# Performance work log

Measured on AMD Instinct MI355X. Metric: run time of the kernel, lower is better.

## Reference

```python
import jax, jax.numpy as jnp
import numpy as np

N_NODES = 20000
N_EDGES = 320000
D = 128  # d_edge = d_node = d_global


def setup_inputs() -> dict:
    key = jax.random.key(0)
    ks = jax.random.split(key, 8)
    inv = lambda fan_in: 1.0 / np.sqrt(fan_in)
    return {
        "edge_attr": jax.random.normal(ks[0], (N_EDGES, D), dtype=jnp.float32),
        "node_attr": jax.random.normal(ks[1], (N_NODES, D), dtype=jnp.float32),
        "u": jax.random.normal(ks[2], (D,), dtype=jnp.float32),
        "senders": jax.random.randint(ks[3], (N_EDGES,), 0, N_NODES, dtype=jnp.int32),
        "receivers": jax.random.randint(ks[4], (N_EDGES,), 0, N_NODES, dtype=jnp.int32),
        "We": jax.random.normal(ks[5], (4 * D, D), dtype=jnp.float32) * inv(4 * D),
        "be": jnp.zeros((D,), dtype=jnp.float32),
        "Wv": jax.random.normal(ks[6], (3 * D, D), dtype=jnp.float32) * inv(3 * D),
        "bv": jnp.zeros((D,), dtype=jnp.float32),
        "Wu": jax.random.normal(ks[7], (3 * D, D), dtype=jnp.float32) * inv(3 * D),
        "bu": jnp.zeros((D,), dtype=jnp.float32),
    }


def reference(edge_attr, node_attr, u, senders, receivers, We, be, Wv, bv, Wu, bu):
    E = edge_attr.shape[0]
    N = node_attr.shape[0]
    u_e = jnp.broadcast_to(u, (E, u.shape[0]))
    u_v = jnp.broadcast_to(u, (N, u.shape[0]))

    # Edge block: phi_e(e, v_r, v_s, u) -- gather endpoint features per edge
    e_in = jnp.concatenate(
        [edge_attr, node_attr[receivers], node_attr[senders], u_e], axis=-1
    )  # [E, 4D]
    e_new = jax.nn.relu(e_in @ We + be)  # [E, D]

    # rho_ev: sum incoming edges per receiver node (scatter-add)
    aggr_e = jax.ops.segment_sum(e_new, receivers, num_segments=N)  # [N, D]

    # Node block: phi_v(aggr_e, v, u)
    v_in = jnp.concatenate([aggr_e, node_attr, u_v], axis=-1)  # [N, 3D]
    v_new = jax.nn.relu(v_in @ Wv + bv)  # [N, D]

    # Global block: rho_eu / rho_vu = mean, phi_u(aggr_e, aggr_v, u)
    aggr_e_u = jnp.mean(e_new, axis=0)
    aggr_v_u = jnp.mean(v_new, axis=0)
    u_in = jnp.concatenate([aggr_e_u, aggr_v_u, u], axis=-1)  # [3D]
    u_new = jax.nn.relu(u_in @ Wu + bu)  # [D]

    return e_new, v_new, u_new
```

## Files before the change

### kernel.cpp

```cpp
#include <hip/hip_runtime.h>
#include <hip/hip_bf16.h>


#define NN 20000
#define NE 320000
#define DD 128
#define SAS 136
#define SBS 136

typedef unsigned short u16;
typedef __attribute__((ext_vector_type(8))) short bf16x8;
typedef __attribute__((ext_vector_type(4))) float f32x4;

__device__ __forceinline__ float b2f(unsigned short h) {
  return __uint_as_float(((unsigned int)h) << 16);
}
__device__ __forceinline__ unsigned short f2b(float f) {
  unsigned int u = __float_as_uint(f);
  unsigned int r = (u + 0x7fffu + ((u >> 16) & 1u)) >> 16;
  return (unsigned short)r;
}

__global__ void k_const(const float* u, const float* We, const float* be,
                        const float* Wv, const float* bv, float* ce,
                        float* cv) {
  __shared__ float su[DD];
  int j = threadIdx.x;
  su[j] = u[j];
  __syncthreads();
  float a = be[j];
  float b = bv[j];
  for (int k = 0; k < DD; ++k) {
    a = fmaf(su[k], We[(384 + k) * DD + j], a);
    b = fmaf(su[k], Wv[(256 + k) * DD + j], b);
  }
  ce[j] = a;
  cv[j] = b;
}

__global__ void k_prep(const float* We, const float* Wv, u16* wt) {
  int m = blockIdx.x;
  const float* W = (m == 0)   ? We
                   : (m == 1) ? We + 128 * DD
                   : (m == 2) ? We + 256 * DD
                   : (m == 3) ? Wv + 128 * DD
                              : Wv;
  u16* o = wt + (size_t)m * DD * DD;
  for (int i = threadIdx.x; i < DD * DD; i += 256) {
    int k = i >> 7, n = i & 127;
    o[n * DD + k] = f2b(W[i]);
  }
}

__global__ void k_hist(const int* recv, int* counts) {
  int e = blockIdx.x * blockDim.x + threadIdx.x;
  if (e < NE) atomicAdd(&counts[recv[e]], 1);
}

__global__ void k_scan(const int* counts, int* rowptr, int* cursor) {
  __shared__ int wsum[16];
  __shared__ int carry;
  int tid = threadIdx.x;
  int lane = tid & 63, wv = tid >> 6;
  if (tid == 0) carry = 0;
  __syncthreads();
  for (int base = 0; base < NN; base += 1024) {
    int i = base + tid;
    int v = (i < NN) ? counts[i] : 0;
    int x = v;
    for (int off = 1; off < 64; off <<= 1) {
      int t = __shfl_up(x, off);
      if (lane >= off) x += t;
    }
    if (lane == 63) wsum[wv] = x;
    __syncthreads();
    if (wv == 0 && lane < 16) {
      int y = wsum[lane];
      for (int off = 1; off < 16; off <<= 1) {
        int t = __shfl_up(y, off);
        if (lane >= off) y += t;
      }
      wsum[lane] = y;
    }
    __syncthreads();
    int woff = (wv > 0) ? wsum[wv - 1] : 0;
    int excl = carry + woff + (x - v);
    if (i < NN) {
      rowptr[i] = excl;
      cursor[i] = excl;
    }
    __syncthreads();
    if (tid == 0) carry += wsum[15];
    __syncthreads();
  }
  if (tid == 0) rowptr[NN] = carry;
}

__global__ void k_fill(const int* recv, int* cursor, int* elist) {
  int e = blockIdx.x * blockDim.x + threadIdx.x;
  if (e < NE) {
    int slot = atomicAdd(&cursor[recv[e]], 1);
    elist[slot] = e;
  }
}

__device__ __forceinline__ void mfma_core(const u16* sA, const u16* sBT,
                                          int lane, int w, f32x4 acc[4][2]) {
  int r15 = lane & 15;
  int koff = (lane >> 4) * 8;
#pragma unroll
  for (int k0 = 0; k0 < DD; k0 += 32) {
    bf16x8 a[4], b[2];
#pragma unroll
    for (int mt = 0; mt < 4; ++mt)
      a[mt] = *(const bf16x8*)&sA[(mt * 16 + r15) * SAS + k0 + koff];
#pragma unroll
    for (int nt = 0; nt < 2; ++nt)
      b[nt] = *(const bf16x8*)&sBT[(w * 32 + nt * 16 + r15) * SBS + k0 + koff];
#pragma unroll
    for (int mt = 0; mt < 4; ++mt)
#pragma unroll
      for (int nt = 0; nt < 2; ++nt)
        acc[mt][nt] = __builtin_amdgcn_mfma_f32_16x16x32_bf16(
            a[mt], b[nt], acc[mt][nt], 0, 0, 0);
  }
}

__device__ __forceinline__ void stage_w(u16* sBT, const u16* wsrc, int tid) {
  const uint4* ws = (const uint4*)wsrc;
  for (int i = tid; i < DD * DD / 8; i += 256) {
    int n = i >> 4, kk = (i & 15) * 8;
    *(uint4*)&sBT[n * SBS + kk] = ws[i];
  }
}

__global__ __launch_bounds__(256) void k_edge(const float* edge_attr,
                                              const u16* wt, const int* recv,
                                              const int* send, const u16* P,
                                              const float* ce, float* e_out,
                                              float* sum_e) {
  __shared__ __align__(16) u16 sA[64 * SAS];
  __shared__ __align__(16) u16 sBT[DD * SBS];
  __shared__ int sRecv[64], sSend[64];
  __shared__ float sCol[DD];
  int tid = threadIdx.x;
  int e0 = blockIdx.x * 64;
  stage_w(sBT, wt, tid);
  const float4* src = (const float4*)(edge_attr + (size_t)e0 * DD);
  for (int i = tid; i < 64 * DD / 4; i += 256) {
    float4 a4 = src[i];
    int rr = i >> 5, cc = (i & 31) * 4;
    ushort4 h;
    h.x = f2b(a4.x); h.y = f2b(a4.y); h.z = f2b(a4.z); h.w = f2b(a4.w);
    *(ushort4*)&sA[rr * SAS + cc] = h;
  }
  if (tid < 64) {
    sRecv[tid] = recv[e0 + tid];
    sSend[tid] = send[e0 + tid];
  }
  if (tid < DD) sCol[tid] = 0.f;
  __syncthreads();
  int lane = tid & 63, w = tid >> 6;
  f32x4 acc[4][2] = {};
  mfma_core(sA, sBT, lane, w, acc);
  int c15 = lane & 15, quad = lane >> 4;
  int col0 = w * 32 + c15, col1 = col0 + 16;
  float ce0 = ce[col0], ce1 = ce[col1];
  float cs0 = 0.f, cs1 = 0.f;
#pragma unroll
  for (int mt = 0; mt < 4; ++mt) {
#pragma unroll
    for (int r = 0; r < 4; ++r) {
      int m = mt * 16 + quad * 4 + r;
      int rc = sRecv[m], sd = sSend[m];
      const u16* p1 = &P[(size_t)rc * 384];
      const u16* p2 = &P[(size_t)sd * 384 + 128];
      float v0 = fmaxf(acc[mt][0][r] + b2f(p1[col0]) + b2f(p2[col0]) + ce0, 0.f);
      float v1 = fmaxf(acc[mt][1][r] + b2f(p1[col1]) + b2f(p2[col1]) + ce1, 0.f);
      size_t ob = (size_t)(e0 + m) * DD;
      e_out[ob + col0] = v0;
      e_out[ob + col1] = v1;
      cs0 += v0;
      cs1 += v1;
    }
  }
  atomicAdd(&sCol[col0], cs0);
  atomicAdd(&sCol[col1], cs1);
  __syncthreads();
  if (tid < DD) atomicAdd(&sum_e[tid], sCol[tid]);
}

__global__ __launch_bounds__(256) void k_nodeproj(const float* node_attr,
                                                  const u16* wt, u16* P) {
  __shared__ __align__(16) u16 sA[64 * SAS];
  __shared__ __align__(16) u16 sBT[DD * SBS];
  int tid = threadIdx.x;
  int n0 = blockIdx.x * 64;
  int sel = blockIdx.y;
  stage_w(sBT, wt + (size_t)(1 + sel) * DD * DD, tid);
  for (int i = tid; i < 64 * DD / 4; i += 256) {
    int rr = i >> 5, cc = (i & 31) * 4;
    float4 a4 = (n0 + rr < NN)
                    ? ((const float4*)node_attr)[(size_t)(n0 + rr) * 32 + (i & 31)]
                    : make_float4(0, 0, 0, 0);
    ushort4 h;
    h.x = f2b(a4.x); h.y = f2b(a4.y); h.z = f2b(a4.z); h.w = f2b(a4.w);
    *(ushort4*)&sA[rr * SAS + cc] = h;
  }
  __syncthreads();
  int lane = tid & 63, w = tid >> 6;
  f32x4 acc[4][2] = {};
  mfma_core(sA, sBT, lane, w, acc);
  int c15 = lane & 15, quad = lane >> 4;
  int col0 = w * 32 + c15, col1 = col0 + 16;
#pragma unroll
  for (int mt = 0; mt < 4; ++mt) {
#pragma unroll
    for (int r = 0; r < 4; ++r) {
      int n = n0 + mt * 16 + quad * 4 + r;
      if (n < NN) {
        u16* o = &P[(size_t)n * 384 + sel * 128];
        o[col0] = f2b(acc[mt][0][r]);
        o[col1] = f2b(acc[mt][1][r]);
      }
    }
  }
}

__global__ __launch_bounds__(256) void k_aggr(const float* e_new,
                                              const int* rowptr,
                                              const int* elist, float* aggr) {
  int tid = threadIdx.x;
  int wv = tid >> 6, lane = tid & 63;
  int n = blockIdx.x * 4 + wv;
  if (n >= NN) return;
  int b = rowptr[n], e = rowptr[n + 1];
  float sx = 0.f, sy = 0.f, tx = 0.f, ty = 0.f;
  int i = b;
  for (; i + 1 < e; i += 2) {
    int e1 = elist[i], e2 = elist[i + 1];
    float2 a = *(const float2*)&e_new[(size_t)e1 * DD + lane * 2];
    float2 c = *(const float2*)&e_new[(size_t)e2 * DD + lane * 2];
    sx += a.x; sy += a.y; tx += c.x; ty += c.y;
  }
  if (i < e) {
    float2 a = *(const float2*)&e_new[(size_t)elist[i] * DD + lane * 2];
    sx += a.x; sy += a.y;
  }
  float2 out;
  out.x = sx + tx;
  out.y = sy + ty;
  *(float2*)&aggr[(size_t)n * DD + lane * 2] = out;
}

__global__ __launch_bounds__(256) void k_node(const float* aggr, const u16* wt,
                                              const u16* P, const float* cv,
                                              float* v_out, float* sum_v) {
  __shared__ __align__(16) u16 sA[64 * SAS];
  __shared__ __align__(16) u16 sBT[DD * SBS];
  __shared__ float sCol[DD];
  int tid = threadIdx.x;
  int n0 = blockIdx.x * 64;
  stage_w(sBT, wt + (size_t)4 * DD * DD, tid);
  for (int i = tid; i < 64 * DD / 4; i += 256) {
    int rr = i >> 5, cc = (i & 31) * 4;
    float4 a4 = (n0 + rr < NN)
                    ? ((const float4*)aggr)[(size_t)(n0 + rr) * 32 + (i & 31)]
                    : make_float4(0, 0, 0, 0);
    ushort4 h;
    h.x = f2b(a4.x); h.y = f2b(a4.y); h.z = f2b(a4.z); h.w = f2b(a4.w);
    *(ushort4*)&sA[rr * SAS + cc] = h;
  }
  if (tid < DD) sCol[tid] = 0.f;
  __syncthreads();
  int lane = tid & 63, w = tid >> 6;
  f32x4 acc[4][2] = {};
  mfma_core(sA, sBT, lane, w, acc);
  int c15 = lane & 15, quad = lane >> 4;
  int col0 = w * 32 + c15, col1 = col0 + 16;
  float cv0 = cv[col0], cv1 = cv[col1];
  float cs0 = 0.f, cs1 = 0.f;
#pragma unroll
  for (int mt = 0; mt < 4; ++mt) {
#pragma unroll
    for (int r = 0; r < 4; ++r) {
      int n = n0 + mt * 16 + quad * 4 + r;
      if (n < NN) {
        const u16* pv = &P[(size_t)n * 384 + 256];
        float v0 = fmaxf(acc[mt][0][r] + b2f(pv[col0]) + cv0, 0.f);
        float v1 = fmaxf(acc[mt][1][r] + b2f(pv[col1]) + cv1, 0.f);
        size_t ob = (size_t)n * DD;
        v_out[ob + col0] = v0;
        v_out[ob + col1] = v1;
        cs0 += v0;
        cs1 += v1;
      }
    }
  }
  atomicAdd(&sCol[col0], cs0);
  atomicAdd(&sCol[col1], cs1);
  __syncthreads();
  if (tid < DD) atomicAdd(&sum_v[tid], sCol[tid]);
}

__global__ void k_global(const float* sumbuf, const float* u, const float* Wu,
                         const float* bu, float* out) {
  __shared__ float sin_[384];
  int j = threadIdx.x;
  sin_[j] = sumbuf[j] * (1.0f / (float)NE);
  sin_[128 + j] = sumbuf[128 + j] * (1.0f / (float)NN);
  sin_[256 + j] = u[j];
  __syncthreads();
  float a = bu[j];
  for (int k = 0; k < 384; ++k) a = fmaf(sin_[k], Wu[k * DD + j], a);
  out[j] = fmaxf(a, 0.f);
}

extern "C" void kernel_launch(void* const* d_in, const int* in_sizes, int n_in,
                              void* d_out, int out_size, void* d_ws,
                              size_t ws_size, hipStream_t stream) {
  const float* edge_attr = (const float*)d_in[0];
  const float* node_attr = (const float*)d_in[1];
  const float* u = (const float*)d_in[2];
  const int* senders = (const int*)d_in[3];
  const int* receivers = (const int*)d_in[4];
  const float* We = (const float*)d_in[5];
  const float* be = (const float*)d_in[6];
  const float* Wv = (const float*)d_in[7];
  const float* bv = (const float*)d_in[8];
  const float* Wu = (const float*)d_in[9];
  const float* bu = (const float*)d_in[10];

  float* e_out = (float*)d_out;
  float* v_out = e_out + (size_t)NE * DD;
  float* u_out = v_out + (size_t)NN * DD;

  int* counts = (int*)d_ws;
  float* sumbuf = (float*)d_ws + NN;
  int* rowptr = (int*)d_ws + NN + 256;
  int* cursor = rowptr + NN + 1;
  int* elist = cursor + NN;
  size_t off = (size_t)(NN + 256 + (NN + 1) + NN + NE);
  off = (off + 3) & ~(size_t)3;
  u16* wt = (u16*)((float*)d_ws + off);
  u16* P = wt + (size_t)5 * DD * DD;
  float* ce = (float*)(P + (size_t)NN * 384);
  float* cv = ce + 128;
  float* aggr = cv + 128;

  hipMemsetAsync(d_ws, 0, (size_t)(NN + 256) * 4, stream);
  k_prep<<<5, 256, 0, stream>>>(We, Wv, wt);
  k_const<<<1, 128, 0, stream>>>(u, We, be, Wv, bv, ce, cv);
  k_hist<<<NE / 256, 256, 0, stream>>>(receivers, counts);
  k_scan<<<1, 1024, 0, stream>>>(counts, rowptr, cursor);
  k_fill<<<NE / 256, 256, 0, stream>>>(receivers, cursor, elist);
  k_nodeproj<<<dim3((NN + 63) / 64, 3), 256, 0, stream>>>(node_attr, wt, P);
  k_edge<<<NE / 64, 256, 0, stream>>>(edge_attr, wt, receivers, senders, P, ce,
                                      e_out, sumbuf);
  k_aggr<<<(NN + 3) / 4, 256, 0, stream>>>(e_out, rowptr, elist, aggr);
  k_node<<<(NN + 63) / 64, 256, 0, stream>>>(aggr, wt, P, cv, v_out,
                                             sumbuf + 128);
  k_global<<<1, 128, 0, stream>>>(sumbuf, u, Wu, bu, u_out);
}
```

Measured before the change: 570.3 us.

## Fuse edge aggregation into persistent receiver-sorted edge kernel and merge setup launches

The edge kernel becomes persistent with a fixed grid. It processes edges in receiver-sorted order through the CSR edge list, prefetching the next tile's gathered inputs into registers while the current tile runs its MFMAs. Segment sums are accumulated as run-length reductions per receiver with global atomics, which removes the separate aggregation pass that re-read all of e_out. Setup, histogram, fill and node-projection launches are merged into fewer kernels. The trade-offs are gathered, non-contiguous edge_attr reads and e_out writes, float atomics that make the sums order-nondeterministic, aggregation of bf16-rounded edge values, and a larger memset for the aggr buffer.

Result: faster. 519.3 us (-9.0%).

```diff
diff --git a/kernel.cpp b/kernel.cpp
--- a/kernel.cpp
+++ b/kernel.cpp
@@ -7,6 +7,8 @@
 #define DD 128
 #define SAS 136
 #define SBS 136
+#define NBLK 768
+#define NTILE 5000
 
 typedef unsigned short u16;
 typedef __attribute__((ext_vector_type(8))) short bf16x8;
@@ -21,40 +23,70 @@
   return (unsigned short)r;
 }
 
-__global__ void k_const(const float* u, const float* We, const float* be,
-                        const float* Wv, const float* bv, float* ce,
-                        float* cv) {
+__device__ __forceinline__ void mfma_core(const u16* sA, const u16* sBT,
+                                          int lane, int w, f32x4 acc[4][2]) {
+  int r15 = lane & 15;
+  int koff = (lane >> 4) * 8;
+#pragma unroll
+  for (int k0 = 0; k0 < DD; k0 += 32) {
+    bf16x8 a[4], b[2];
+#pragma unroll
+    for (int mt = 0; mt < 4; ++mt)
+      a[mt] = *(const bf16x8*)&sA[(mt * 16 + r15) * SAS + k0 + koff];
+#pragma unroll
+    for (int nt = 0; nt < 2; ++nt)
+      b[nt] = *(const bf16x8*)&sBT[(w * 32 + nt * 16 + r15) * SBS + k0 + koff];
+#pragma unroll
+    for (int mt = 0; mt < 4; ++mt)
+#pragma unroll
+      for (int nt = 0; nt < 2; ++nt)
+        acc[mt][nt] = __builtin_amdgcn_mfma_f32_16x16x32_bf16(
+            a[mt], b[nt], acc[mt][nt], 0, 0, 0);
+  }
+}
+
+__device__ __forceinline__ void stage_w(u16* sBT, const u16* wsrc, int tid) {
+  const uint4* ws = (const uint4*)wsrc;
+  for (int i = tid; i < DD * DD / 8; i += 256) {
+    int n = i >> 4, kk = (i & 15) * 8;
+    *(uint4*)&sBT[n * SBS + kk] = ws[i];
+  }
+}
+
+__global__ __launch_bounds__(256) void k_setup(const int* recv, int* counts,
+                                               const float* We, const float* Wv,
+                                               const float* u, const float* be,
+                                               const float* bv, u16* wt,
+                                               float* ce, float* cv) {
   __shared__ float su[DD];
-  int j = threadIdx.x;
-  su[j] = u[j];
-  __syncthreads();
-  float a = be[j];
-  float b = bv[j];
-  for (int k = 0; k < DD; ++k) {
-    a = fmaf(su[k], We[(384 + k) * DD + j], a);
-    b = fmaf(su[k], Wv[(256 + k) * DD + j], b);
-  }
-  ce[j] = a;
-  cv[j] = b;
-}
-
-__global__ void k_prep(const float* We, const float* Wv, u16* wt) {
-  int m = blockIdx.x;
-  const float* W = (m == 0)   ? We
-                   : (m == 1) ? We + 128 * DD
-                   : (m == 2) ? We + 256 * DD
-                   : (m == 3) ? Wv + 128 * DD
-                              : Wv;
-  u16* o = wt + (size_t)m * DD * DD;
-  for (int i = threadIdx.x; i < DD * DD; i += 256) {
-    int k = i >> 7, n = i & 127;
-    o[n * DD + k] = f2b(W[i]);
-  }
-}
-
-__global__ void k_hist(const int* recv, int* counts) {
-  int e = blockIdx.x * blockDim.x + threadIdx.x;
-  if (e < NE) atomicAdd(&counts[recv[e]], 1);
+  int b = blockIdx.x, tid = threadIdx.x;
+  if (b < 1250) {
+    atomicAdd(&counts[recv[b * 256 + tid]], 1);
+  } else if (b < 1255) {
+    int m = b - 1250;
+    const float* W = (m == 0)   ? We
+                     : (m == 1) ? We + 128 * DD
+                     : (m == 2) ? We + 256 * DD
+                     : (m == 3) ? Wv + 128 * DD
+                                : Wv;
+    u16* o = wt + (size_t)m * DD * DD;
+    for (int i = tid; i < DD * DD; i += 256) {
+      int k = i >> 7, n = i & 127;
+      o[n * DD + k] = f2b(W[i]);
+    }
+  } else {
+    if (tid < DD) su[tid] = u[tid];
+    __syncthreads();
+    if (tid < DD) {
+      float a = be[tid], c = bv[tid];
+      for (int k = 0; k < DD; ++k) {
+        a = fmaf(su[k], We[(384 + k) * DD + tid], a);
+        c = fmaf(su[k], Wv[(256 + k) * DD + tid], c);
+      }
+      ce[tid] = a;
+      cv[tid] = c;
+    }
+  }
 }
 
 __global__ void k_scan(const int* counts, int* rowptr, int* cursor) {
@@ -96,108 +128,19 @@
   if (tid == 0) rowptr[NN] = carry;
 }
 
-__global__ void k_fill(const int* recv, int* cursor, int* elist) {
-  int e = blockIdx.x * blockDim.x + threadIdx.x;
-  if (e < NE) {
+__global__ __launch_bounds__(256) void k_mid(const int* recv, int* cursor,
+                                             int* elist, const float* node_attr,
+                                             const u16* wt, u16* P) {
+  __shared__ __align__(16) u16 sA[64 * SAS];
+  __shared__ __align__(16) u16 sBT[DD * SBS];
+  int b = blockIdx.x, tid = threadIdx.x;
+  if (b < 1250) {
+    int e = b * 256 + tid;
     int slot = atomicAdd(&cursor[recv[e]], 1);
     elist[slot] = e;
-  }
-}
-
-__device__ __forceinline__ void mfma_core(const u16* sA, const u16* sBT,
-                                          int lane, int w, f32x4 acc[4][2]) {
-  int r15 = lane & 15;
-  int koff = (lane >> 4) * 8;
-#pragma unroll
-  for (int k0 = 0; k0 < DD; k0 += 32) {
-    bf16x8 a[4], b[2];
-#pragma unroll
-    for (int mt = 0; mt < 4; ++mt)
-      a[mt] = *(const bf16x8*)&sA[(mt * 16 + r15) * SAS + k0 + koff];
-#pragma unroll
-    for (int nt = 0; nt < 2; ++nt)
-      b[nt] = *(const bf16x8*)&sBT[(w * 32 + nt * 16 + r15) * SBS + k0 + koff];
-#pragma unroll
-    for (int mt = 0; mt < 4; ++mt)
-#pragma unroll
-      for (int nt = 0; nt < 2; ++nt)
-        acc[mt][nt] = __builtin_amdgcn_mfma_f32_16x16x32_bf16(
-            a[mt], b[nt], acc[mt][nt], 0, 0, 0);
-  }
-}
-
-__device__ __forceinline__ void stage_w(u16* sBT, const u16* wsrc, int tid) {
-  const uint4* ws = (const uint4*)wsrc;
-  for (int i = tid; i < DD * DD / 8; i += 256) {
-    int n = i >> 4, kk = (i & 15) * 8;
-    *(uint4*)&sBT[n * SBS + kk] = ws[i];
-  }
-}
-
-__global__ __launch_bounds__(256) void k_edge(const float* edge_attr,
-                                              const u16* wt, const int* recv,
-                                              const int* send, const u16* P,
-                                              const float* ce, float* e_out,
-                                              float* sum_e) {
-  __shared__ __align__(16) u16 sA[64 * SAS];
-  __shared__ __align__(16) u16 sBT[DD * SBS];
-  __shared__ int sRecv[64], sSend[64];
-  __shared__ float sCol[DD];
-  int tid = threadIdx.x;
-  int e0 = blockIdx.x * 64;
-  stage_w(sBT, wt, tid);
-  const float4* src = (const float4*)(edge_attr + (size_t)e0 * DD);
-  for (int i = tid; i < 64 * DD / 4; i += 256) {
-    float4 a4 = src[i];
-    int rr = i >> 5, cc = (i & 31) * 4;
-    ushort4 h;
-    h.x = f2b(a4.x); h.y = f2b(a4.y); h.z = f2b(a4.z); h.w = f2b(a4.w);
-    *(ushort4*)&sA[rr * SAS + cc] = h;
-  }
-  if (tid < 64) {
-    sRecv[tid] = recv[e0 + tid];
-    sSend[tid] = send[e0 + tid];
-  }
-  if (tid < DD) sCol[tid] = 0.f;
-  __syncthreads();
-  int lane = tid & 63, w = tid >> 6;
-  f32x4 acc[4][2] = {};
-  mfma_core(sA, sBT, lane, w, acc);
-  int c15 = lane & 15, quad = lane >> 4;
-  int col0 = w * 32 + c15, col1 = col0 + 16;
-  float ce0 = ce[col0], ce1 = ce[col1];
-  float cs0 = 0.f, cs1 = 0.f;
-#pragma unroll
-  for (int mt = 0; mt < 4; ++mt) {
-#pragma unroll
-    for (int r = 0; r < 4; ++r) {
-      int m = mt * 16 + quad * 4 + r;
-      int rc = sRecv[m], sd = sSend[m];
-      const u16* p1 = &P[(size_t)rc * 384];
-      const u16* p2 = &P[(size_t)sd * 384 + 128];
-      float v0 = fmaxf(acc[mt][0][r] + b2f(p1[col0]) + b2f(p2[col0]) + ce0, 0.f);
-      float v1 = fmaxf(acc[mt][1][r] + b2f(p1[col1]) + b2f(p2[col1]) + ce1, 0.f);
-      size_t ob = (size_t)(e0 + m) * DD;
-      e_out[ob + col0] = v0;
-      e_out[ob + col1] = v1;
-      cs0 += v0;
-      cs1 += v1;
-    }
-  }
-  atomicAdd(&sCol[col0], cs0);
-  atomicAdd(&sCol[col1], cs1);
-  __syncthreads();
-  if (tid < DD) atomicAdd(&sum_e[tid], sCol[tid]);
-}
-
-__global__ __launch_bounds__(256) void k_nodeproj(const float* node_attr,
-                                                  const u16* wt, u16* P) {
-  __shared__ __align__(16) u16 sA[64 * SAS];
-  __shared__ __align__(16) u16 sBT[DD * SBS];
-  int tid = threadIdx.x;
-  int n0 = blockIdx.x * 64;
-  int sel = blockIdx.y;
-  stage_w(sBT, wt + (size_t)(1 + sel) * DD * DD, tid);
+    return;
+  }
+  int n0 = (b - 1250) * 64;
   for (int i = tid; i < 64 * DD / 4; i += 256) {
     int rr = i >> 5, cc = (i & 31) * 4;
     float4 a4 = (n0 + rr < NN)
@@ -207,50 +150,158 @@
     h.x = f2b(a4.x); h.y = f2b(a4.y); h.z = f2b(a4.z); h.w = f2b(a4.w);
     *(ushort4*)&sA[rr * SAS + cc] = h;
   }
-  __syncthreads();
   int lane = tid & 63, w = tid >> 6;
-  f32x4 acc[4][2] = {};
-  mfma_core(sA, sBT, lane, w, acc);
   int c15 = lane & 15, quad = lane >> 4;
   int col0 = w * 32 + c15, col1 = col0 + 16;
-#pragma unroll
-  for (int mt = 0; mt < 4; ++mt) {
-#pragma unroll
-    for (int r = 0; r < 4; ++r) {
-      int n = n0 + mt * 16 + quad * 4 + r;
-      if (n < NN) {
-        u16* o = &P[(size_t)n * 384 + sel * 128];
-        o[col0] = f2b(acc[mt][0][r]);
-        o[col1] = f2b(acc[mt][1][r]);
-      }
-    }
-  }
-}
-
-__global__ __launch_bounds__(256) void k_aggr(const float* e_new,
-                                              const int* rowptr,
-                                              const int* elist, float* aggr) {
+  for (int sel = 0; sel < 3; ++sel) {
+    __syncthreads();
+    stage_w(sBT, wt + (size_t)(1 + sel) * DD * DD, tid);
+    __syncthreads();
+    f32x4 acc[4][2] = {};
+    mfma_core(sA, sBT, lane, w, acc);
+#pragma unroll
+    for (int mt = 0; mt < 4; ++mt)
+#pragma unroll
+      for (int r = 0; r < 4; ++r) {
+        int n = n0 + mt * 16 + quad * 4 + r;
+        if (n < NN) {
+          u16* o = &P[(size_t)n * 384 + sel * 128];
+          o[col0] = f2b(acc[mt][0][r]);
+          o[col1] = f2b(acc[mt][1][r]);
+        }
+      }
+  }
+}
+
+__global__ __launch_bounds__(256) void k_edge(const float* edge_attr,
+                                              const u16* wt, const int* elist,
+                                              const int* recv, const int* send,
+                                              const u16* P, const float* ce,
+                                              float* e_out, float* aggr,
+                                              float* sum_e) {
+  __shared__ __align__(16) u16 sBT[DD * SBS];
+  __shared__ __align__(16) u16 sAO[64 * SAS];
+  __shared__ int sEid[64], sRecv[64], sSend[64];
   int tid = threadIdx.x;
-  int wv = tid >> 6, lane = tid & 63;
-  int n = blockIdx.x * 4 + wv;
-  if (n >= NN) return;
-  int b = rowptr[n], e = rowptr[n + 1];
-  float sx = 0.f, sy = 0.f, tx = 0.f, ty = 0.f;
-  int i = b;
-  for (; i + 1 < e; i += 2) {
-    int e1 = elist[i], e2 = elist[i + 1];
-    float2 a = *(const float2*)&e_new[(size_t)e1 * DD + lane * 2];
-    float2 c = *(const float2*)&e_new[(size_t)e2 * DD + lane * 2];
-    sx += a.x; sy += a.y; tx += c.x; ty += c.y;
-  }
-  if (i < e) {
-    float2 a = *(const float2*)&e_new[(size_t)elist[i] * DD + lane * 2];
-    sx += a.x; sy += a.y;
-  }
-  float2 out;
-  out.x = sx + tx;
-  out.y = sy + ty;
-  *(float2*)&aggr[(size_t)n * DD + lane * 2] = out;
+  int lane = tid & 63, w = tid >> 6;
+  int r15 = lane & 15, quad = lane >> 4;
+  int col0 = w * 32 + r15, col1 = col0 + 16;
+  int myrow = tid >> 5;
+  int mycol = (tid & 31) * 4;
+
+  float4 areg[8];
+  int eid8[8];
+  int eidN = 0, rcN = 0, sdN = 0;
+  int t = blockIdx.x;
+
+  {
+    int base = t * 64;
+#pragma unroll
+    for (int j = 0; j < 8; ++j) eid8[j] = elist[base + myrow + 8 * j];
+    if (tid < 64) {
+      eidN = elist[base + tid];
+      rcN = recv[eidN];
+      sdN = send[eidN];
+    }
+#pragma unroll
+    for (int j = 0; j < 8; ++j)
+      areg[j] = *(const float4*)&edge_attr[(size_t)eid8[j] * DD + mycol];
+  }
+  stage_w(sBT, wt, tid);
+  float ce0 = ce[col0], ce1 = ce[col1];
+  float colsum = 0.f;
+  bool first = true;
+
+  for (; t < NTILE; t += NBLK) {
+    if (!first) __syncthreads();
+    first = false;
+#pragma unroll
+    for (int j = 0; j < 8; ++j) {
+      ushort4 h;
+      h.x = f2b(areg[j].x); h.y = f2b(areg[j].y);
+      h.z = f2b(areg[j].z); h.w = f2b(areg[j].w);
+      *(ushort4*)&sAO[(myrow + 8 * j) * SAS + mycol] = h;
+    }
+    if (tid < 64) {
+      sEid[tid] = eidN;
+      sRecv[tid] = rcN;
+      sSend[tid] = sdN;
+    }
+    __syncthreads();
+    int tn = t + NBLK;
+    if (tn < NTILE) {
+      int base = tn * 64;
+#pragma unroll
+      for (int j = 0; j < 8; ++j) eid8[j] = elist[base + myrow + 8 * j];
+      if (tid < 64) {
+        eidN = elist[base + tid];
+        rcN = recv[eidN];
+        sdN = send[eidN];
+      }
+#pragma unroll
+      for (int j = 0; j < 8; ++j)
+        areg[j] = *(const float4*)&edge_attr[(size_t)eid8[j] * DD + mycol];
+    }
+    f32x4 acc[4][2] = {};
+    mfma_core(sAO, sBT, lane, w, acc);
+    float vv[4][2][4];
+#pragma unroll
+    for (int mt = 0; mt < 4; ++mt)
+#pragma unroll
+      for (int r = 0; r < 4; ++r) {
+        int m = mt * 16 + quad * 4 + r;
+        const u16* p1 = &P[(size_t)sRecv[m] * 384];
+        const u16* p2 = &P[(size_t)sSend[m] * 384 + 128];
+        vv[mt][0][r] =
+            fmaxf(acc[mt][0][r] + b2f(p1[col0]) + b2f(p2[col0]) + ce0, 0.f);
+        vv[mt][1][r] =
+            fmaxf(acc[mt][1][r] + b2f(p1[col1]) + b2f(p2[col1]) + ce1, 0.f);
+      }
+    __syncthreads();
+    u16* sOutH = sAO;
+#pragma unroll
+    for (int mt = 0; mt < 4; ++mt)
+#pragma unroll
+      for (int r = 0; r < 4; ++r) {
+        int m = mt * 16 + quad * 4 + r;
+        sOutH[m * SAS + col0] = f2b(vv[mt][0][r]);
+        sOutH[m * SAS + col1] = f2b(vv[mt][1][r]);
+      }
+    __syncthreads();
+    if (tid < DD) {
+      float run = 0.f;
+      int prev = sRecv[0];
+      for (int r = 0; r < 64; ++r) {
+        int cur = sRecv[r];
+        float v = b2f(sOutH[r * SAS + tid]);
+        if (cur != prev) {
+          atomicAdd(&aggr[(size_t)prev * DD + tid], run);
+          run = 0.f;
+          prev = cur;
+        }
+        run += v;
+        colsum += v;
+      }
+      atomicAdd(&aggr[(size_t)prev * DD + tid], run);
+    } else {
+      int tt = tid - 128;
+#pragma unroll
+      for (int j = 0; j < 8; ++j) {
+        int i = tt + 128 * j;
+        int row = i >> 4, ch = (i & 15) * 8;
+        uint4 q = *(const uint4*)&sOutH[row * SAS + ch];
+        float4 f0, f1;
+        f0.x = b2f((u16)(q.x & 0xffff)); f0.y = b2f((u16)(q.x >> 16));
+        f0.z = b2f((u16)(q.y & 0xffff)); f0.w = b2f((u16)(q.y >> 16));
+        f1.x = b2f((u16)(q.z & 0xffff)); f1.y = b2f((u16)(q.z >> 16));
+        f1.z = b2f((u16)(q.w & 0xffff)); f1.w = b2f((u16)(q.w >> 16));
+        float* dst = &e_out[(size_t)sEid[row] * DD + ch];
+        *(float4*)dst = f0;
+        *(float4*)(dst + 4) = f1;
+      }
+    }
+  }
+  if (tid < DD) atomicAdd(&sum_e[tid], colsum);
 }
 
 __global__ __launch_bounds__(256) void k_node(const float* aggr, const u16* wt,
@@ -281,7 +332,7 @@
   float cv0 = cv[col0], cv1 = cv[col1];
   float cs0 = 0.f, cs1 = 0.f;
 #pragma unroll
-  for (int mt = 0; mt < 4; ++mt) {
+  for (int mt = 0; mt < 4; ++mt)
 #pragma unroll
     for (int r = 0; r < 4; ++r) {
       int n = n0 + mt * 16 + quad * 4 + r;
@@ -296,7 +347,6 @@
         cs1 += v1;
       }
     }
-  }
   atomicAdd(&sCol[col0], cs0);
   atomicAdd(&sCol[col1], cs1);
   __syncthreads();
@@ -337,27 +387,25 @@
 
   int* counts = (int*)d_ws;
   float* sumbuf = (float*)d_ws + NN;
-  int* rowptr = (int*)d_ws + NN + 256;
+  float* aggr = (float*)d_ws + NN + 256;
+  int* rowptr = (int*)d_ws + NN + 256 + NN * DD;
   int* cursor = rowptr + NN + 1;
   int* elist = cursor + NN;
-  size_t off = (size_t)(NN + 256 + (NN + 1) + NN + NE);
+  size_t off = (size_t)(NN + 256 + NN * DD + (NN + 1) + NN + NE);
   off = (off + 3) & ~(size_t)3;
   u16* wt = (u16*)((float*)d_ws + off);
   u16* P = wt + (size_t)5 * DD * DD;
   float* ce = (float*)(P + (size_t)NN * 384);
   float* cv = ce + 128;
-  float* aggr = cv + 128;
-
-  hipMemsetAsync(d_ws, 0, (size_t)(NN + 256) * 4, stream);
-  k_prep<<<5, 256, 0, stream>>>(We, Wv, wt);
-  k_const<<<1, 128, 0, stream>>>(u, We, be, Wv, bv, ce, cv);
-  k_hist<<<NE / 256, 256, 0, stream>>>(receivers, counts);
+
+  hipMemsetAsync(d_ws, 0, (size_t)(NN + 256 + NN * DD) * 4, stream);
+  k_setup<<<1256, 256, 0, stream>>>(receivers, counts, We, Wv, u, be, bv, wt,
+                                    ce, cv);
   k_scan<<<1, 1024, 0, stream>>>(counts, rowptr, cursor);
-  k_fill<<<NE / 256, 256, 0, stream>>>(receivers, cursor, elist);
-  k_nodeproj<<<dim3((NN + 63) / 64, 3), 256, 0, stream>>>(node_attr, wt, P);
-  k_edge<<<NE / 64, 256, 0, stream>>>(edge_attr, wt, receivers, senders, P, ce,
-                                      e_out, sumbuf);
-  k_aggr<<<(NN + 3) / 4, 256, 0, stream>>>(e_out, rowptr, elist, aggr);
+  k_mid<<<1250 + 313, 256, 0, stream>>>(receivers, cursor, elist, node_attr,
+                                        wt, P);
+  k_edge<<<NBLK, 256, 0, stream>>>(edge_attr, wt, elist, receivers, senders, P,
+                                   ce, e_out, aggr, sumbuf);
   k_node<<<(NN + 63) / 64, 256, 0, stream>>>(aggr, wt, P, cv, v_out,
                                              sumbuf + 128);
   k_global<<<1, 128, 0, stream>>>(sumbuf, u, Wu, bu, u_out);
```
